# Performance work log

Hardware: AMD Instinct MI355X
Metric: run time of the kernel (lower is better)

Reference implementation:

```python
import jax, jax.numpy as jnp
import numpy as np

DIM = 2
N_SIGMA = 2
H, W = 1024, 2048


def setup_inputs() -> dict:
    key = jax.random.key(0)
    p = jax.random.normal(key, (1, DIM + N_SIGMA + 3, H, W), dtype=jnp.float32)
    # temper sigma channels so s = exp(10*sigma) is O(1): large proposals, few loop iters
    p = p.at[0, DIM:DIM + N_SIGMA].set(p[0, DIM:DIM + N_SIGMA] * 0.03 - 0.05)
    return {"prediction": p}


def _cluster(prediction, n_sigma=2, threshold=0.5, min_pixel=160, min_inst_pixel=160,
             min_seed_thresh=0.5, inst_ratio=0.5, dist_thresh=0.5):
    pred = prediction[0]                      # [C, H, W]
    h, w = pred.shape[1], pred.shape[2]
    n = h * w
    # coordinate grid (xym sliced to [0:h, 0:w])
    x = jnp.linspace(0.0, 2.0, 2048)[:w]
    y = jnp.linspace(0.0, 1.0, 1024)[:h]
    xym = jnp.stack([jnp.broadcast_to(x[None, :], (h, w)),
                     jnp.broadcast_to(y[:, None], (h, w))], axis=0)      # [2, h, w]

    spatial_emb = (jnp.tanh(pred[:DIM]) + xym).reshape(DIM, n)           # [2, N]
    sigma = pred[DIM:DIM + n_sigma].reshape(n_sigma, n)                  # [ns, N]
    seed = jax.nn.sigmoid(pred[DIM + 2 + n_sigma]).reshape(n)            # [N]

    mask = seed > min_seed_thresh                                        # [N] bool
    # instead of gathering masked pixels into a ragged array, keep full N and
    # restrict every proposal to the mask (same math, jit-compatible shapes)
    init = (mask, jnp.zeros((n,), jnp.int32), jnp.int32(1), jnp.array(False))

    def cond(carry):
        uncl, inst, count, stop = carry
        return jnp.logical_and(~stop, uncl.sum() > min_pixel)

    def body(carry):
        uncl, inst, count, stop = carry
        scores = seed * uncl                                             # [N]
        sidx = jnp.argmax(scores)
        sscore = scores[sidx]
        go = sscore >= threshold                                         # break if below
        center = spatial_emb[:, sidx]                                    # [2]
        s = jnp.exp(sigma[:, sidx] * 10.0)                               # [ns]
        dist = jnp.exp(-jnp.sum((spatial_emb - center[:, None]) ** 2 * s[:, None], axis=0))
        proposal = jnp.logical_and(dist > dist_thresh, mask)             # [N]
        uncl2 = uncl.at[sidx].set(False)
        psum = proposal.sum()
        ratio = (uncl2 & proposal).sum().astype(jnp.float32) / jnp.maximum(psum, 1).astype(jnp.float32)
        accept = go & (psum > min_inst_pixel) & (ratio > inst_ratio)
        inst_new = jnp.where(accept, jnp.where(proposal, count, inst), inst)
        count_new = count + accept.astype(jnp.int32)
        uncl_new = jnp.where(go, uncl2 & ~proposal, uncl)
        return (uncl_new, inst_new, count_new, ~go)

    _, inst, _, _ = jax.lax.while_loop(cond, body, init)
    return inst.reshape(1, h, w).astype(jnp.uint8)


def reference(prediction):
    return _cluster(prediction)
```

## Files before the change

### kernel.cpp

```cpp
#include <hip/hip_runtime.h>

typedef unsigned long long u64;

#define HH 1024
#define WW 2048
#define NN (HH*WW)
#define GRID 256
#define BLOCK 512
#define PXT 16
#define CHUNK (PXT*BLOCK)

struct Coord {
  u64 A[2][GRID];
  u64 B[2][GRID];
  u64 pub[2][8];
};

__device__ __forceinline__ float sigmoid_ref(float x) {
  #pragma clang fp contract(off)
  return 0.5f + 0.5f * tanhf(0.5f * x);
}

__device__ __forceinline__ void slot_store(u64* p, u64 v) {
  __hip_atomic_store(p, v, __ATOMIC_RELAXED, __HIP_MEMORY_SCOPE_AGENT);
}
__device__ __forceinline__ u64 slot_load(u64* p) {
  return __hip_atomic_load(p, __ATOMIC_RELAXED, __HIP_MEMORY_SCOPE_AGENT);
}

__device__ void barrier_exchange(Coord* __restrict__ c, const float* __restrict__ pred,
                                 int b, int t, int tok,
                                 float bv, int bi, int lu, int lps, int lin,
                                 int& sidx, int& un, int& go, int& acc,
                                 float& cx, float& cy, float& s0, float& s1)
{
  #pragma clang fp contract(off)
  __shared__ u64 wA[8], wS[8];
  __shared__ int wU[8];
  __shared__ u64 pubsh;
  const int par = tok & 1, w = t >> 6, lane = t & 63;
  const u64 tg = (u64)(unsigned)(tok & 0xFFF);

  unsigned fb = 0; int ic = 0;
  if (bv >= 0.0f) { fb = __float_as_uint(bv); ic = bi; }
  u64 am = ((u64)fb << 21) | (u64)(unsigned)(NN - 1 - ic);
  u64 sm = ((u64)(unsigned)lps << 42) | ((u64)(unsigned)lin << 21) | (u64)(unsigned)lu;
  for (int off = 32; off; off >>= 1) {
    u64 o = __shfl_xor(am, off); if (o > am) am = o;
    sm += __shfl_xor(sm, off);
  }
  if (lane == 0) { wA[w] = am; wS[w] = sm; }
  __syncthreads();
  if (t == 0) {
    u64 A0 = wA[0], S0 = wS[0];
    #pragma unroll
    for (int j = 1; j < 8; ++j) { if (wA[j] > A0) A0 = wA[j]; S0 += wS[j]; }
    slot_store(&c->A[par][b], (tg << 52) | A0);
    slot_store(&c->B[par][b], (tg << 52) | ((S0 >> 42) << 28) |
                              (((S0 >> 21) & 0x3FFFull) << 14) | (S0 & 0x3FFFull));
  }
  __syncthreads();

  if (b == 0) {
    u64 got;
    if (t < GRID) {
      u64* p = &c->A[par][t];
      while (((got = slot_load(p)) >> 52) != tg) __builtin_amdgcn_s_sleep(1);
      got &= (1ull << 52) - 1;
      for (int off = 32; off; off >>= 1) { u64 o = __shfl_xor(got, off); if (o > got) got = o; }
      if (lane == 0) wA[w] = got;
    } else {
      u64* p = &c->B[par][t - GRID];
      while (((got = slot_load(p)) >> 52) != tg) __builtin_amdgcn_s_sleep(1);
      int lp = (int)((got >> 28) & 0x3FFFull);
      int ln = (int)((got >> 14) & 0x3FFFull);
      int lq = (int)(got & 0x3FFFull);
      u64 pk = ((u64)(unsigned)lp << 32) | (unsigned)ln;
      for (int off = 32; off; off >>= 1) { pk += __shfl_xor(pk, off); lq += __shfl_xor(lq, off); }
      if (lane == 0) { wS[w] = pk; wU[w] = lq; }
    }
    __syncthreads();
    if (t == 0) {
      u64 A0 = wA[0];
      #pragma unroll
      for (int j = 1; j < 4; ++j) if (wA[j] > A0) A0 = wA[j];
      u64 PK = wS[4] + wS[5] + wS[6] + wS[7];
      int UN = wU[4] + wU[5] + wU[6] + wU[7];
      int psum = (int)(PK >> 32), inter = (int)(PK & 0xFFFFFFFFull);
      int idx = NN - 1 - (int)(A0 & 0x1FFFFFull);
      float sv = __uint_as_float((unsigned)(A0 >> 21));
      int g = (sv >= 0.5f) ? 1 : 0;
      int a = (psum > 160 && 2 * inter > psum) ? 1 : 0;
      u64 pb = (tg << 52) | ((u64)(unsigned)g << 44) | ((u64)(unsigned)a << 43) |
               ((u64)(unsigned)UN << 21) | (u64)(unsigned)idx;
      slot_store(&c->pub[par][0], pb);
      pubsh = pb;
    }
    __syncthreads();
  } else {
    if (t == 0) {
      u64 v;
      while (((v = slot_load(&c->pub[par][0])) >> 52) != tg) __builtin_amdgcn_s_sleep(1);
      pubsh = v;
    }
    __syncthreads();
  }

  u64 v = pubsh;
  sidx = (int)(v & 0x1FFFFFull);
  un   = (int)((v >> 21) & 0x3FFFFFull);
  acc  = (int)((v >> 43) & 1ull);
  go   = (int)((v >> 44) & 1ull);
  cx = tanhf(pred[sidx])      + (2.0f / 2047.0f) * (float)(sidx & (WW - 1));
  cy = tanhf(pred[NN + sidx]) + (1.0f / 1023.0f) * (float)(sidx >> 11);
  s0 = expf(pred[2 * NN + sidx] * 10.0f);
  s1 = expf(pred[3 * NN + sidx] * 10.0f);
}

__global__ void init_kernel(Coord* c) {
  int t = blockIdx.x * blockDim.x + threadIdx.x;
  u64* p = (u64*)c;
  int n = (int)(sizeof(Coord) / 8);
  if (t < n) p[t] = 0;
}

__global__ __launch_bounds__(BLOCK, 1)
void cluster_kernel(const float* __restrict__ pred,
                    int* __restrict__ out,
                    Coord* __restrict__ c)
{
  #pragma clang fp contract(off)
  const int b = blockIdx.x, t = threadIdx.x;
  const int base = b * CHUNK;

  const float xstep = 2.0f / 2047.0f;
  const float ystep = 1.0f / 1023.0f;

  float ex[PXT], ey[PXT], sd[PXT];
  unsigned mbits = 0, ubits;
  float bv = -1.0f; int bi = 0; int mc = 0;
  #pragma unroll
  for (int k = 0; k < PXT; ++k) {
    int i = base + t + k * BLOCK;
    float seed = sigmoid_ref(pred[6 * NN + i]);
    sd[k] = seed;
    unsigned m = (seed > 0.5f) ? 1u : 0u;
    mbits |= m << k;
    ex[k] = tanhf(pred[i])      + xstep * (float)(i & (WW - 1));
    ey[k] = tanhf(pred[NN + i]) + ystep * (float)(i >> 11);
    out[i] = 0;
    mc += (int)m;
    float scv = m ? seed : 0.0f;
    if (scv > bv) { bv = scv; bi = i; }
  }
  ubits = mbits;

  int sidx, un, go, acc; float cx, cy, s0, s1;
  int tok = 1;
  barrier_exchange(c, pred, b, t, tok, bv, bi, mc, 0, 0,
                   sidx, un, go, acc, cx, cy, s0, s1); tok++;

  int count = 1;
  unsigned prev_pr = 0;
  for (int it = 0; it < 4000; ++it) {
    if (it && acc) {
      #pragma unroll
      for (int k = 0; k < PXT; ++k)
        if ((prev_pr >> k) & 1u) out[base + t + k * BLOCK] = count;
      count++;
    }
    if (un <= 160) break;
    if (!go) break;

    int rel = sidx - base;
    unsigned sbit = 0;
    if (rel >= 0 && rel < CHUNK && (rel & (BLOCK - 1)) == t)
      sbit = 1u << (rel >> 9);

    unsigned pr = 0;
    #pragma unroll
    for (int k = 0; k < PXT; ++k) {
      float dx = ex[k] - cx, dy = ey[k] - cy;
      float dsq = (dx * dx) * s0 + (dy * dy) * s1;
      float dist = expf(-dsq);
      pr |= ((dist > 0.5f) ? 1u : 0u) << k;
    }
    pr &= mbits;
    int lps = __popc(pr);
    int lin = __popc(pr & ubits & ~sbit);
    ubits &= ~pr; ubits &= ~sbit;
    int lu = __popc(ubits);

    bv = -1.0f; bi = 0;
    #pragma unroll
    for (int k = 0; k < PXT; ++k) {
      if (((ubits >> k) & 1u) && sd[k] > bv) { bv = sd[k]; bi = base + t + k * BLOCK; }
    }
    prev_pr = pr;
    barrier_exchange(c, pred, b, t, tok, bv, bi, lu, lps, lin,
                     sidx, un, go, acc, cx, cy, s0, s1); tok++;
  }
}

extern "C" void kernel_launch(void* const* d_in, const int* in_sizes, int n_in,
                              void* d_out, int out_size, void* d_ws, size_t ws_size,
                              hipStream_t stream) {
  const float* pred = (const float*)d_in[0];
  int* out = (int*)d_out;
  Coord* c = (Coord*)d_ws;

  init_kernel<<<dim3((unsigned)((sizeof(Coord)/8 + 255)/256)), dim3(256), 0, stream>>>(c);

  cluster_kernel<<<dim3(GRID), dim3(BLOCK), 0, stream>>>(pred, out, c);
}
```

Baseline: 69.82 us.

## Replicate broadcast slot per wave and vectorize contiguous pixel ownership

```diff
diff --git a/kernel.cpp b/kernel.cpp
--- a/kernel.cpp
+++ b/kernel.cpp
@@ -13,7 +13,7 @@
 struct Coord {
   u64 A[2][GRID];
   u64 B[2][GRID];
-  u64 pub[2][8];
+  u64 pub[2][8][16];
 };
 
 __device__ __forceinline__ float sigmoid_ref(float x) {
@@ -37,7 +37,6 @@
   #pragma clang fp contract(off)
   __shared__ u64 wA[8], wS[8];
   __shared__ int wU[8];
-  __shared__ u64 pubsh;
   const int par = tok & 1, w = t >> 6, lane = t & 63;
   const u64 tg = (u64)(unsigned)(tok & 0xFFF);
 
@@ -93,20 +92,17 @@
       int a = (psum > 160 && 2 * inter > psum) ? 1 : 0;
       u64 pb = (tg << 52) | ((u64)(unsigned)g << 44) | ((u64)(unsigned)a << 43) |
                ((u64)(unsigned)UN << 21) | (u64)(unsigned)idx;
-      slot_store(&c->pub[par][0], pb);
-      pubsh = pb;
-    }
-    __syncthreads();
-  } else {
-    if (t == 0) {
-      u64 v;
-      while (((v = slot_load(&c->pub[par][0])) >> 52) != tg) __builtin_amdgcn_s_sleep(1);
-      pubsh = v;
-    }
-    __syncthreads();
-  }
-
-  u64 v = pubsh;
+      #pragma unroll
+      for (int r = 0; r < 8; ++r) slot_store(&c->pub[par][r][0], pb);
+    }
+  }
+
+  u64 v = 0;
+  if (lane == 0) {
+    u64* p = &c->pub[par][w & 7][0];
+    while (((v = slot_load(p)) >> 52) != tg) __builtin_amdgcn_s_sleep(1);
+  }
+  v = __shfl(v, 0);
   sidx = (int)(v & 0x1FFFFFull);
   un   = (int)((v >> 21) & 0x3FFFFFull);
   acc  = (int)((v >> 43) & 1ull);
@@ -132,6 +128,7 @@
   #pragma clang fp contract(off)
   const int b = blockIdx.x, t = threadIdx.x;
   const int base = b * CHUNK;
+  const int i0 = base + t * PXT;
 
   const float xstep = 2.0f / 2047.0f;
   const float ystep = 1.0f / 1023.0f;
@@ -140,18 +137,33 @@
   unsigned mbits = 0, ubits;
   float bv = -1.0f; int bi = 0; int mc = 0;
   #pragma unroll
-  for (int k = 0; k < PXT; ++k) {
-    int i = base + t + k * BLOCK;
-    float seed = sigmoid_ref(pred[6 * NN + i]);
-    sd[k] = seed;
-    unsigned m = (seed > 0.5f) ? 1u : 0u;
-    mbits |= m << k;
-    ex[k] = tanhf(pred[i])      + xstep * (float)(i & (WW - 1));
-    ey[k] = tanhf(pred[NN + i]) + ystep * (float)(i >> 11);
-    out[i] = 0;
-    mc += (int)m;
-    float scv = m ? seed : 0.0f;
-    if (scv > bv) { bv = scv; bi = i; }
+  for (int j = 0; j < 4; ++j) {
+    float4 v0 = *reinterpret_cast<const float4*>(&pred[i0 + 4 * j]);
+    float4 v1 = *reinterpret_cast<const float4*>(&pred[NN + i0 + 4 * j]);
+    float4 v6 = *reinterpret_cast<const float4*>(&pred[6 * NN + i0 + 4 * j]);
+    #pragma unroll
+    for (int e = 0; e < 4; ++e) {
+      const int k = 4 * j + e;
+      const int i = i0 + k;
+      float p0 = (e == 0) ? v0.x : (e == 1) ? v0.y : (e == 2) ? v0.z : v0.w;
+      float p1 = (e == 0) ? v1.x : (e == 1) ? v1.y : (e == 2) ? v1.z : v1.w;
+      float p6 = (e == 0) ? v6.x : (e == 1) ? v6.y : (e == 2) ? v6.z : v6.w;
+      float seed = sigmoid_ref(p6);
+      sd[k] = seed;
+      unsigned m = (seed > 0.5f) ? 1u : 0u;
+      mbits |= m << k;
+      ex[k] = tanhf(p0) + xstep * (float)(i & (WW - 1));
+      ey[k] = tanhf(p1) + ystep * (float)(i >> 11);
+      mc += (int)m;
+      float scv = m ? seed : 0.0f;
+      if (scv > bv) { bv = scv; bi = i; }
+    }
+  }
+  {
+    int4 z = make_int4(0, 0, 0, 0);
+    #pragma unroll
+    for (int j = 0; j < 4; ++j)
+      *reinterpret_cast<int4*>(&out[i0 + 4 * j]) = z;
   }
   ubits = mbits;
 
@@ -166,7 +178,7 @@
     if (it && acc) {
       #pragma unroll
       for (int k = 0; k < PXT; ++k)
-        if ((prev_pr >> k) & 1u) out[base + t + k * BLOCK] = count;
+        if ((prev_pr >> k) & 1u) out[i0 + k] = count;
       count++;
     }
     if (un <= 160) break;
@@ -174,8 +186,7 @@
 
     int rel = sidx - base;
     unsigned sbit = 0;
-    if (rel >= 0 && rel < CHUNK && (rel & (BLOCK - 1)) == t)
-      sbit = 1u << (rel >> 9);
+    if ((rel >> 4) == t) sbit = 1u << (rel & 15);
 
     unsigned pr = 0;
     #pragma unroll
@@ -194,7 +205,7 @@
     bv = -1.0f; bi = 0;
     #pragma unroll
     for (int k = 0; k < PXT; ++k) {
-      if (((ubits >> k) & 1u) && sd[k] > bv) { bv = sd[k]; bi = base + t + k * BLOCK; }
+      if (((ubits >> k) & 1u) && sd[k] > bv) { bv = sd[k]; bi = i0 + k; }
     }
     prev_pr = pr;
     barrier_exchange(c, pred, b, t, tok, bv, bi, lu, lps, lin,
```

Measured after the change: 66.61 us. 1.05x faster.
